# Performance work log

Measured on AMD Instinct MI355X. Metric: run time of the kernel, lower is better.

The kernel has to match this reference:

```python
import jax, jax.numpy as jnp
import numpy as np

B, S, H = 2, 2048, 4096
NH, NKV, HD = 32, 8, 128
THETA = 1000000.0
NEG = jnp.finfo(jnp.float32).min


def setup_inputs() -> dict:
    key = jax.random.key(0)
    ks = jax.random.split(key, 9)
    s = 0.02
    return {
        "hidden_states": jax.random.normal(ks[0], (B, S, H), jnp.float32),
        "position_ids": jnp.tile(jnp.arange(S, dtype=jnp.int32)[None, :], (B, 1)),
        "Wq": jax.random.normal(ks[1], (NH * HD, H), jnp.float32) * s,
        "bq": jax.random.normal(ks[2], (NH * HD,), jnp.float32) * s,
        "Wk": jax.random.normal(ks[3], (NKV * HD, H), jnp.float32) * s,
        "bk": jax.random.normal(ks[4], (NKV * HD,), jnp.float32) * s,
        "Wv": jax.random.normal(ks[5], (NKV * HD, H), jnp.float32) * s,
        "bv": jax.random.normal(ks[6], (NKV * HD,), jnp.float32) * s,
        "Wo": jax.random.normal(ks[7], (H, H), jnp.float32) * s,
        "bo": jax.random.normal(ks[8], (H,), jnp.float32) * s,
    }


def _rotate_half_interleaved(x):
    # y[..., ::2] = -x[..., 1::2]; y[..., 1::2] = x[..., ::2]
    x2 = x.reshape(*x.shape[:-1], -1, 2)
    y = jnp.stack([-x2[..., 1], x2[..., 0]], axis=-1)
    return y.reshape(x.shape)


def reference(hidden_states, position_ids, Wq, bq, Wk, bk, Wv, bv, Wo, bo):
    bsz, q_len, _ = hidden_states.shape
    q = (hidden_states @ Wq.T + bq).reshape(bsz, q_len, NH, HD).transpose(0, 2, 1, 3)
    k = (hidden_states @ Wk.T + bk).reshape(bsz, q_len, NKV, HD).transpose(0, 2, 1, 3)
    v = (hidden_states @ Wv.T + bv).reshape(bsz, q_len, NKV, HD).transpose(0, 2, 1, 3)

    # rotary embedding (interleaved / repeat_interleave variant)
    inv_freq = 1.0 / (THETA ** (jnp.arange(0, HD, 2, dtype=jnp.float32) / HD))
    freqs = position_ids.astype(jnp.float32)[:, :, None] * inv_freq[None, None, :]  # [B,S,HD/2]
    emb = jnp.repeat(freqs, 2, axis=-1)  # [B,S,HD]
    cos = jnp.cos(emb)[:, None, :, :]  # [B,1,S,HD]
    sin = jnp.sin(emb)[:, None, :, :]
    q = q * cos + _rotate_half_interleaved(q) * sin
    k = k * cos + _rotate_half_interleaved(k) * sin

    # GQA: repeat KV heads (repeat_interleave on head axis)
    n_rep = NH // NKV
    k = jnp.repeat(k, n_rep, axis=1)
    v = jnp.repeat(v, n_rep, axis=1)

    scores = jnp.einsum("bhqd,bhkd->bhqk", q, k) / np.sqrt(HD).astype(np.float32)
    causal = jnp.tril(jnp.ones((q_len, q_len), dtype=bool))
    scores = jnp.where(causal[None, None, :, :], scores, NEG)
    attn = jax.nn.softmax(scores.astype(jnp.float32), axis=-1).astype(q.dtype)
    out = jnp.einsum("bhqk,bhkd->bhqd", attn, v)
    out = out.transpose(0, 2, 1, 3).reshape(bsz, q_len, H)
    return out @ Wo.T + bo
```

## Files before the change

### kernel.cpp

```cpp
#include <hip/hip_runtime.h>
#include <stdint.h>

typedef __bf16 bf16x8 __attribute__((ext_vector_type(8)));
typedef float f32x4 __attribute__((ext_vector_type(4)));
typedef float f32x16 __attribute__((ext_vector_type(16)));

#define S_LEN 2048
#define NKVH 8
#define HDIM 128
#define MROWS 4096
#define LDQKV 6144
#define SCALE 0.08838834764831845f
#define C_LOG2 0.1275405707067851f
#define THR_RAW 62.7f
#define ROPE_L2 0.31143075889569023f

__device__ __forceinline__ unsigned short f2bf(float f) {
  unsigned u = __float_as_uint(f);
  u += 0x7FFFu + ((u >> 16) & 1u);
  return (unsigned short)(u >> 16);
}
__device__ __forceinline__ float bf2f(unsigned short h) {
  return __uint_as_float(((unsigned)h) << 16);
}

__device__ __forceinline__ void gload16(const unsigned short* g, unsigned short* l) {
  __builtin_amdgcn_global_load_lds(
      (__attribute__((address_space(1))) void*)(g),
      (__attribute__((address_space(3))) void*)(l), 16, 0, 0);
}

__global__ void cast4(const float4* __restrict__ s0, const float4* __restrict__ s1,
                      const float4* __restrict__ s2, const float4* __restrict__ s3,
                      ushort4* __restrict__ d0, ushort4* __restrict__ d1,
                      ushort4* __restrict__ d2, ushort4* __restrict__ d3) {
  const int b = blockIdx.x;
  const float4* s; ushort4* d; int lb;
  if (b < 1024)      { s = s0; d = d0; lb = b; }
  else if (b < 2048) { s = s1; d = d1; lb = b - 1024; }
  else if (b < 2304) { s = s2; d = d2; lb = b - 2048; }
  else               { s = s3; d = d3; lb = b - 2304; }
  int base = lb * 4096 + threadIdx.x;
#pragma unroll
  for (int i = 0; i < 16; i++) {
    float4 v = s[base + i * 256];
    ushort4 o;
    o.x = f2bf(v.x); o.y = f2bf(v.y); o.z = f2bf(v.z); o.w = f2bf(v.w);
    d[base + i * 256] = o;
  }
}

__global__ void cast_f32_bf16(const float4* __restrict__ in, ushort4* __restrict__ out, int n4) {
  int i = blockIdx.x * 256 + threadIdx.x;
  const int stride = gridDim.x * 256;
  for (; i < n4; i += stride) {
    float4 v = in[i];
    ushort4 o;
    o.x = f2bf(v.x); o.y = f2bf(v.y); o.z = f2bf(v.z); o.w = f2bf(v.w);
    out[i] = o;
  }
}

template <int OUTF, int ROPE>
__global__ __launch_bounds__(512, 2)
void gemm256(const unsigned short* __restrict__ A,
             const unsigned short* __restrict__ Bw,
             const float* __restrict__ bias,
             void* __restrict__ C,
             const int* __restrict__ pos,
             int ldc, int K) {
  __shared__ unsigned short lds[8][8192];

  const int t = threadIdx.x;
  const int lane = t & 63;
  const int w = t >> 6;
  const int wr = w >> 2, wc = w & 3;
  const int row16 = lane & 15, kgrp = lane >> 4;
  const int m0 = blockIdx.y * 256, n0 = blockIdx.x * 256;

  const int riu = t >> 3;
  const int col = (((t & 7) ^ (riu & 7)) << 3);
  const int rB0 = (riu & 31) + ((riu >> 5) << 6);
  const unsigned short* pA = A + (size_t)(m0 + riu) * K + col;
  const unsigned short* pB = Bw + (size_t)(n0 + rB0) * K + col;

#define STGU(SL, SRC)                                                       \
  {                                                                         \
    gload16((SRC), &lds[SL][t * 8]);                                        \
    gload16((SRC) + (size_t)128 * K, &lds[SL][4096 + t * 8]);               \
  }
#define RDA(SL)                                                             \
  _Pragma("unroll") for (int mi = 0; mi < 4; mi++)                          \
  _Pragma("unroll") for (int ks = 0; ks < 2; ks++)                          \
    afr[mi][ks] = *(const bf16x8*)(&lds[SL][0] + abase + mi * 1024 +        \
                                   ((((ks << 2) + kgrp) ^ sw) << 3));
#define RDB(SL, W)                                                          \
  _Pragma("unroll") for (int nj = 0; nj < 2; nj++)                          \
  _Pragma("unroll") for (int ks = 0; ks < 2; ks++)                          \
    bfr[W][nj][ks] = *(const bf16x8*)(&lds[SL][0] + bbase + nj * 1024 +     \
                                      ((((ks << 2) + kgrp) ^ sw) << 3));
#define MM(MO, NO, W)                                                       \
  __builtin_amdgcn_s_setprio(1);                                            \
  _Pragma("unroll") for (int mi = 0; mi < 4; mi++)                          \
  _Pragma("unroll") for (int nj = 0; nj < 2; nj++)                          \
  _Pragma("unroll") for (int ks = 0; ks < 2; ks++)                          \
    acc[(MO) + mi][(NO) + nj] = __builtin_amdgcn_mfma_f32_16x16x32_bf16(    \
        afr[mi][ks], bfr[W][nj][ks], acc[(MO) + mi][(NO) + nj], 0, 0, 0);   \
  __builtin_amdgcn_s_setprio(0);
#define BAR __builtin_amdgcn_s_barrier()

  const int sw = row16 & 7;
  const int abase = (wr * 64 + row16) * 64;
  const int bbase = (wc * 32 + row16) * 64;

  f32x4 acc[8][4];
#pragma unroll
  for (int i = 0; i < 8; i++)
#pragma unroll
    for (int j = 0; j < 4; j++) acc[i][j] = (f32x4){0.f, 0.f, 0.f, 0.f};

  bf16x8 afr[4][2], bfr[2][2][2];
  const int NT = K >> 6;
  const int NI = NT >> 1;

  STGU(0, pA);
  STGU(1, pB);
  STGU(2, pB + (size_t)32 * K);
  STGU(3, pA + (size_t)64 * K);
  STGU(4, pA + 64);
  STGU(5, pB + 64);
  STGU(6, pB + (size_t)32 * K + 64);
  asm volatile("s_waitcnt vmcnt(6)" ::: "memory");
  BAR;

  for (int I = 0; I < NI; ++I) {
    const size_t k1 = ((size_t)(2 * I + 1)) << 6;
    const size_t k2 = ((size_t)(2 * I + 2)) << 6;
    const size_t k3 = ((size_t)(2 * I + 3)) << 6;
    const bool s2 = (I + 1 < NI);

    RDA(0); RDB(1, 0);
    STGU(7, pA + (size_t)64 * K + k1);
    BAR;
    MM(0, 0, 0);
    BAR;
    RDB(2, 1);
    if (s2) STGU(0, pA + k2);
    BAR;
    MM(0, 2, 1);
    BAR;
    RDA(3);
    if (s2) STGU(1, pB + k2);
    BAR;
    MM(4, 2, 1);
    BAR;
    if (s2) {
      STGU(2, pB + (size_t)32 * K + k2);
      asm volatile("s_waitcnt vmcnt(6)" ::: "memory");
    } else {
      asm volatile("s_waitcnt vmcnt(0)" ::: "memory");
    }
    BAR;
    MM(4, 0, 0);
    BAR;
    RDA(4); RDB(5, 0);
    if (s2) STGU(3, pA + (size_t)64 * K + k2);
    BAR;
    MM(0, 0, 0);
    BAR;
    RDB(6, 1);
    if (s2) STGU(4, pA + k3);
    BAR;
    MM(0, 2, 1);
    BAR;
    RDA(7);
    if (s2) STGU(5, pB + k3);
    BAR;
    MM(4, 2, 1);
    BAR;
    if (s2) {
      STGU(6, pB + (size_t)32 * K + k3);
      asm volatile("s_waitcnt vmcnt(6)" ::: "memory");
    } else {
      asm volatile("s_waitcnt vmcnt(0)" ::: "memory");
    }
    BAR;
    MM(4, 0, 0);
    BAR;
  }
#undef STGU
#undef RDA
#undef RDB
#undef MM
#undef BAR

#pragma unroll
  for (int MI = 0; MI < 8; MI++) {
#pragma unroll
    for (int NJ = 0; NJ < 4; NJ++) {
      const int gr = m0 + wr * 128 + MI * 16 + kgrp * 4;
      const int gc = n0 + wc * 64 + NJ * 16 + row16;
      const float bv = bias[gc];
      if (ROPE) {
        const int hf = (gc & 127) >> 1;
        const float inv = exp2f(-(float)hf * ROPE_L2);
#pragma unroll
        for (int jj = 0; jj < 4; jj++) {
          float v = acc[MI][NJ][jj] + bv;
          float px = __shfl_xor(v, 1);
          float sn, cs;
          __sincosf((float)pos[gr + jj] * inv, &sn, &cs);
          float ov = (gc & 1) ? fmaf(v, cs, px * sn) : fmaf(v, cs, -px * sn);
          ((unsigned short*)C)[(size_t)(gr + jj) * ldc + gc] = f2bf(ov);
        }
      } else {
#pragma unroll
        for (int jj = 0; jj < 4; jj++) {
          float v = acc[MI][NJ][jj] + bv;
          if (OUTF) ((float*)C)[(size_t)(gr + jj) * ldc + gc] = v;
          else ((unsigned short*)C)[(size_t)(gr + jj) * ldc + gc] = f2bf(v);
        }
      }
    }
  }
}

template <int OUTF, int ROPE>
__global__ __launch_bounds__(512, 2)
void gemm128(const unsigned short* __restrict__ A,
             const unsigned short* __restrict__ Bw,
             const float* __restrict__ bias,
             void* __restrict__ C,
             const int* __restrict__ pos,
             int ldc, int K) {
  __shared__ unsigned short lds[3 * 24576];

  const int t = threadIdx.x;
  const int lane = t & 63;
  const int w = t >> 6;
  const int wr = w >> 2, wc = w & 3;
  const int row16 = lane & 15, kgrp = lane >> 4;
  const int m0 = blockIdx.y * 128, n0 = blockIdx.x * 256;

  const int riu = t >> 3;
  const int col = (((t & 7) ^ (riu & 7)) << 3);
  const unsigned short* pA = A + (size_t)(m0 + riu) * K + col;
  const unsigned short* pB = Bw + (size_t)(n0 + riu) * K + col;

#define STG6(bo_, kk_)                                                      \
  {                                                                         \
    gload16(pA + (kk_), &lds[(bo_) + t * 8]);                               \
    gload16(pA + (size_t)64 * K + (kk_), &lds[(bo_) + 4096 + t * 8]);       \
    gload16(pB + (kk_), &lds[(bo_) + 8192 + t * 8]);                        \
    gload16(pB + (size_t)64 * K + (kk_), &lds[(bo_) + 12288 + t * 8]);      \
    gload16(pB + (size_t)128 * K + (kk_), &lds[(bo_) + 16384 + t * 8]);     \
    gload16(pB + (size_t)192 * K + (kk_), &lds[(bo_) + 20480 + t * 8]);     \
  }

  const int sw = row16 & 7;
  const int abase = (wr * 64 + row16) * 64;
  const int bbase = 8192 + (wc * 64 + row16) * 64;

  f32x4 acc[4][4];
#pragma unroll
  for (int i = 0; i < 4; i++)
#pragma unroll
    for (int j = 0; j < 4; j++) acc[i][j] = (f32x4){0.f, 0.f, 0.f, 0.f};

  bf16x8 afr[4][2], bfr[4][2];
  const int NT = K >> 6;

  STG6(0, 0);
  STG6(24576, 64);

  int rbc = 0;
  int rbs = 2;
  for (int T = 0; T < NT; ++T) {
    if (T < NT - 1) { asm volatile("s_waitcnt vmcnt(6)\n\ts_barrier" ::: "memory"); }
    else            { asm volatile("s_waitcnt vmcnt(0)\n\ts_barrier" ::: "memory"); }
    if (T + 2 < NT) STG6(rbs * 24576, (size_t)(T + 2) << 6);
    const unsigned short* Lc = &lds[rbc * 24576];

#pragma unroll
    for (int mi = 0; mi < 4; mi++)
#pragma unroll
      for (int ks = 0; ks < 2; ks++)
        afr[mi][ks] = *(const bf16x8*)(Lc + abase + mi * 1024 + ((((ks << 2) + kgrp) ^ sw) << 3));
#pragma unroll
    for (int nj = 0; nj < 4; nj++)
#pragma unroll
      for (int ks = 0; ks < 2; ks++)
        bfr[nj][ks] = *(const bf16x8*)(Lc + bbase + nj * 1024 + ((((ks << 2) + kgrp) ^ sw) << 3));

    __builtin_amdgcn_s_setprio(1);
#pragma unroll
    for (int mi = 0; mi < 4; mi++)
#pragma unroll
      for (int nj = 0; nj < 4; nj++)
#pragma unroll
        for (int ks = 0; ks < 2; ks++)
          acc[mi][nj] = __builtin_amdgcn_mfma_f32_16x16x32_bf16(afr[mi][ks], bfr[nj][ks], acc[mi][nj], 0, 0, 0);
    __builtin_amdgcn_s_setprio(0);

    rbc++; if (rbc == 3) rbc = 0;
    rbs++; if (rbs == 3) rbs = 0;
  }
#undef STG6

#pragma unroll
  for (int MI = 0; MI < 4; MI++) {
#pragma unroll
    for (int NJ = 0; NJ < 4; NJ++) {
      const int gr = m0 + wr * 64 + MI * 16 + kgrp * 4;
      const int gc = n0 + wc * 64 + NJ * 16 + row16;
      const float bv = bias[gc];
      if (ROPE && gc < 1024) {
        const int hf = (gc & 127) >> 1;
        const float inv = exp2f(-(float)hf * ROPE_L2);
#pragma unroll
        for (int jj = 0; jj < 4; jj++) {
          float v = acc[MI][NJ][jj] + bv;
          float px = __shfl_xor(v, 1);
          float sn, cs;
          __sincosf((float)pos[gr + jj] * inv, &sn, &cs);
          float ov = (gc & 1) ? fmaf(v, cs, px * sn) : fmaf(v, cs, -px * sn);
          ((unsigned short*)C)[(size_t)(gr + jj) * ldc + gc] = f2bf(ov);
        }
      } else {
#pragma unroll
        for (int jj = 0; jj < 4; jj++) {
          float v = acc[MI][NJ][jj] + bv;
          if (OUTF) ((float*)C)[(size_t)(gr + jj) * ldc + gc] = v;
          else ((unsigned short*)C)[(size_t)(gr + jj) * ldc + gc] = f2bf(v);
        }
      }
    }
  }
}

__global__ void transpose_v(const unsigned short* __restrict__ V, int ldv,
                            unsigned short* __restrict__ Vt) {
  __shared__ unsigned short tile[32][40];
  const int t = threadIdx.x;
  const int n0 = blockIdx.x * 32;
  const int m0 = blockIdx.y * 32;
  const int r = t >> 3;
  const int c = (t & 7) << 2;
  const unsigned short* src = V + (size_t)(m0 + r) * ldv + n0 + c;
  ushort4 d = *(const ushort4*)src;
  tile[r][c] = d.x; tile[r][c + 1] = d.y; tile[r][c + 2] = d.z; tile[r][c + 3] = d.w;
  __syncthreads();
  const int b = m0 >> 11;
  unsigned short* dst = Vt + (size_t)(b * 1024 + n0 + r) * 2048 + (m0 & 2047) + c;
  ushort4 o;
  o.x = tile[c][r]; o.y = tile[c + 1][r]; o.z = tile[c + 2][r]; o.w = tile[c + 3][r];
  *(ushort4*)dst = o;
}

__global__ __launch_bounds__(256, 2)
void attn_kernel3(const unsigned short* __restrict__ QKV,
                  const unsigned short* __restrict__ Vt,
                  unsigned short* __restrict__ O) {
  __shared__ unsigned short sK[2 * 2 * 64 * 64];
  __shared__ unsigned short sV[2 * 128 * 64];

  const int t = threadIdx.x;
  const int lane = t & 63;
  const int w = t >> 6;
  const int l31 = lane & 31;
  const int hi = lane >> 5;
  const int bid = blockIdx.x;
  const int g = bid >> 6, bh = bid & 63;
  const int qt = (g < 8) ? (15 - g) : (g - 8);
  const int b = bh >> 5, h = bh & 31;
  const int kh = h >> 2;
  const int q0 = qt << 7;
  const int qw = q0 + w * 32;
  const int qg = qw + l31;

  const int ntiles = (q0 + 128) >> 6;
  const int myTiles = (qw + 95) >> 6;

  const int kr5 = t >> 3;
  const int ksw2 = ((t & 7) ^ (kr5 & 7)) << 3;
  const int vrow0 = t >> 3;
  const int vslot = t & 7;
  const unsigned short* Kp = QKV + (size_t)(b * S_LEN) * LDQKV + 4096 + kh * HDIM;
  const unsigned short* Vp = Vt + (size_t)(b * 1024 + kh * HDIM) * 2048;
  const int vsw = (vslot ^ (vrow0 & 7)) << 3;
  const unsigned short* KpA = Kp + (size_t)kr5 * LDQKV + ksw2;
  const unsigned short* VpA = Vp + (size_t)vrow0 * 2048 + vsw;

#define STAGE(bufi, kv0m)                                                      \
  {                                                                            \
    _Pragma("unroll")                                                          \
    for (int p = 0; p < 4; p++)                                                \
      gload16(KpA + (size_t)((kv0m) + ((p & 1) << 5)) * LDQKV + ((p >> 1) << 6), \
              &sK[(bufi) * 8192 + p * 2048 + t * 8]);                          \
    _Pragma("unroll")                                                          \
    for (int p = 0; p < 4; p++)                                                \
      gload16(VpA + (kv0m) + p * 65536, &sV[(bufi) * 8192 + p * 2048 + t * 8]); \
  }

  bf16x8 qf[8];
  {
    const unsigned short* qb = QKV + (size_t)(b * S_LEN + qw + l31) * LDQKV + h * HDIM + hi * 8;
#pragma unroll
    for (int kd = 0; kd < 8; kd++) qf[kd] = *(const bf16x8*)(qb + kd * 16);
  }

  f32x16 o[4];
#pragma unroll
  for (int nt = 0; nt < 4; nt++)
#pragma unroll
    for (int r = 0; r < 16; r++) o[nt][r] = 0.f;
  float m = -1e30f, lsum = 0.f;

  const int rw7 = (l31 & 7) << 4;
  const int kswz = (hi << 4) ^ rw7;
  const int kbase = l31 << 6;
  const int vbase = l31 * 64;

  STAGE(0, 0);
  int buf = 0;
  for (int it = 0; it < ntiles; ++it) {
    if (it + 1 < ntiles) {
      STAGE(buf ^ 1, (it + 1) << 6);
      asm volatile("s_waitcnt vmcnt(8)" ::: "memory");
    } else {
      asm volatile("s_waitcnt vmcnt(0)" ::: "memory");
    }
    __builtin_amdgcn_s_barrier();

    if (it < myTiles) {
      const unsigned short* sKc = sK + buf * 8192;
      const unsigned short* sVc = sV + buf * 8192;
      const int kv0 = it << 6;

      f32x16 st[2];
#pragma unroll
      for (int r = 0; r < 16; r++) { st[0][r] = 0.f; st[1][r] = 0.f; }
      __builtin_amdgcn_s_setprio(1);
#pragma unroll
      for (int kd = 0; kd < 8; kd++) {
        const int koff = ((kd >> 2) << 12) + ((((kd & 3) << 5) ^ kswz) >> 1);
        bf16x8 k0 = *(const bf16x8*)(sKc + koff + kbase);
        bf16x8 k1 = *(const bf16x8*)(sKc + koff + kbase + 2048);
        st[0] = __builtin_amdgcn_mfma_f32_32x32x16_bf16(k0, qf[kd], st[0], 0, 0, 0);
        st[1] = __builtin_amdgcn_mfma_f32_32x32x16_bf16(k1, qf[kd], st[1], 0, 0, 0);
      }
      __builtin_amdgcn_s_setprio(0);

      if (it == myTiles - 1) {
#pragma unroll
        for (int s2 = 0; s2 < 2; s2++)
#pragma unroll
          for (int r = 0; r < 16; r++) {
            const int kvg = kv0 + s2 * 32 + (r & 3) + 8 * (r >> 2) + 4 * hi;
            if (kvg > qg) st[s2][r] = -1e30f;
          }
      }

      float mx[8];
#pragma unroll
      for (int r = 0; r < 8; r++)
        mx[r] = fmaxf(fmaxf(st[0][r], st[0][r + 8]), fmaxf(st[1][r], st[1][r + 8]));
#pragma unroll
      for (int d = 4; d >= 1; d >>= 1)
#pragma unroll
        for (int r = 0; r < d; r++) mx[r] = fmaxf(mx[r], mx[r + d]);
      float tmax = fmaxf(mx[0], __shfl_xor(mx[0], 32));

      if (!__all(tmax <= m + THR_RAW)) {
        const float mnew = fmaxf(m, tmax);
        const float corr = exp2f((m - mnew) * C_LOG2);
        lsum *= corr;
#pragma unroll
        for (int r = 0; r < 16; r++) {
          const int src = (r & 3) + 8 * (r >> 2) + 4 * hi;
          const float cr = __shfl(corr, src);
#pragma unroll
          for (int nt = 0; nt < 4; nt++) o[nt][r] *= cr;
        }
        m = mnew;
      }
      const float mC = m * C_LOG2;

#pragma unroll
      for (int s2 = 0; s2 < 2; s2++)
#pragma unroll
        for (int r = 0; r < 16; r++) st[s2][r] = exp2f(fmaf(st[s2][r], C_LOG2, -mC));
      float sm[8];
#pragma unroll
      for (int r = 0; r < 8; r++)
        sm[r] = (st[0][r] + st[0][r + 8]) + (st[1][r] + st[1][r + 8]);
#pragma unroll
      for (int d = 4; d >= 1; d >>= 1)
#pragma unroll
        for (int r = 0; r < d; r++) sm[r] += sm[r + d];
      float tsum = sm[0] + __shfl_xor(sm[0], 32);
      lsum += tsum;

      bf16x8 pa[4];
#pragma unroll
      for (int s2 = 0; s2 < 2; s2++) {
        unsigned pw[8];
#pragma unroll
        for (int i = 0; i < 8; i++)
          asm("v_cvt_pk_bf16_f32 %0, %1, %2" : "=v"(pw[i]) : "v"(st[s2][2 * i]), "v"(st[s2][2 * i + 1]));
        const unsigned y0 = hi ? pw[0] : pw[2];
        const unsigned y1 = hi ? pw[1] : pw[3];
        const unsigned y2 = hi ? pw[4] : pw[6];
        const unsigned y3 = hi ? pw[5] : pw[7];
        const unsigned x0 = (unsigned)__shfl_xor((int)y0, 32);
        const unsigned x1 = (unsigned)__shfl_xor((int)y1, 32);
        const unsigned x2 = (unsigned)__shfl_xor((int)y2, 32);
        const unsigned x3 = (unsigned)__shfl_xor((int)y3, 32);
        union { unsigned u[4]; bf16x8 v; } u0, u1;
        u0.u[0] = hi ? x0 : pw[0];
        u0.u[1] = hi ? x1 : pw[1];
        u0.u[2] = hi ? pw[2] : x0;
        u0.u[3] = hi ? pw[3] : x1;
        u1.u[0] = hi ? x2 : pw[4];
        u1.u[1] = hi ? x3 : pw[5];
        u1.u[2] = hi ? pw[6] : x2;
        u1.u[3] = hi ? pw[7] : x3;
        pa[2 * s2] = u0.v; pa[2 * s2 + 1] = u1.v;
      }

      __builtin_amdgcn_s_setprio(1);
#pragma unroll
      for (int nt = 0; nt < 4; nt++) {
        const unsigned short* vr = sVc + vbase + nt * 2048;
#pragma unroll
        for (int ks = 0; ks < 4; ks++) {
          bf16x8 vb = *(const bf16x8*)(vr + (((ks << 5) ^ kswz) >> 1));
          o[nt] = __builtin_amdgcn_mfma_f32_32x32x16_bf16(pa[ks], vb, o[nt], 0, 0, 0);
        }
      }
      __builtin_amdgcn_s_setprio(0);
    }

    __builtin_amdgcn_s_barrier();
    buf ^= 1;
  }

  const float linv = 1.0f / lsum;
#pragma unroll
  for (int r = 0; r < 16; r++) {
    const int qr = (r & 3) + 8 * (r >> 2) + 4 * hi;
    const float lr = __shfl(linv, qr);
    unsigned short* orow = O + (size_t)(b * S_LEN + qw + qr) * 4096 + h * HDIM + l31;
#pragma unroll
    for (int nt = 0; nt < 4; nt++) orow[nt * 32] = f2bf(o[nt][r] * lr);
  }
#undef STAGE
}

extern "C" void kernel_launch(void* const* d_in, const int* in_sizes, int n_in,
                              void* d_out, int out_size, void* d_ws, size_t ws_size,
                              hipStream_t stream) {
  const float* hs = (const float*)d_in[0];
  const int*  pos = (const int*)d_in[1];
  const float* Wq = (const float*)d_in[2];
  const float* bq = (const float*)d_in[3];
  const float* Wk = (const float*)d_in[4];
  const float* bk = (const float*)d_in[5];
  const float* Wv = (const float*)d_in[6];
  const float* bv = (const float*)d_in[7];
  const float* Wo = (const float*)d_in[8];
  const float* bo = (const float*)d_in[9];
  float* out = (float*)d_out;

  char* ws = (char*)d_ws;
  unsigned short* hbf  = (unsigned short*)(ws);
  unsigned short* Wbuf = (unsigned short*)(ws + 33554432);
  unsigned short* QKV  = (unsigned short*)(ws + 83886080);
  unsigned short* Vtb  = (unsigned short*)(ws + 134217728);
  float*          biasb= (float*)(ws + 142606336);

  cast4<<<2560, 256, 0, stream>>>(
      (const float4*)hs, (const float4*)Wq, (const float4*)Wk, (const float4*)Wv,
      (ushort4*)hbf, (ushort4*)Wbuf, (ushort4*)(Wbuf + 16777216), (ushort4*)(Wbuf + 20971520));
  hipMemcpyAsync(biasb, bq, 4096 * 4, hipMemcpyDeviceToDevice, stream);
  hipMemcpyAsync(biasb + 4096, bk, 1024 * 4, hipMemcpyDeviceToDevice, stream);
  hipMemcpyAsync(biasb + 5120, bv, 1024 * 4, hipMemcpyDeviceToDevice, stream);

  gemm256<0, 1><<<dim3(16, 16), 512, 0, stream>>>(hbf, Wbuf, biasb, QKV, pos, LDQKV, 4096);
  gemm128<0, 1><<<dim3(8, 32), 512, 0, stream>>>(hbf, Wbuf + 16777216, biasb + 4096, QKV + 4096, pos, LDQKV, 4096);

  cast_f32_bf16<<<2048, 256, 0, stream>>>((const float4*)Wo, (ushort4*)Wbuf, 4194304);

  transpose_v<<<dim3(32, 128), 256, 0, stream>>>(QKV + 5120, LDQKV, Vtb);

  attn_kernel3<<<dim3(1024), 256, 0, stream>>>(QKV, Vtb, hbf);

  gemm256<1, 0><<<dim3(16, 16), 512, 0, stream>>>(hbf, Wbuf, bo, out, nullptr, 4096, 4096);
}
```

Measured before the change: 507.0 us.

## Widen attention KV tile to 128 and drop double-buffered prefetch

The attention kernel now processes 128 keys per iteration instead of 64, using four score accumulators and eight PV k-steps, which halves the loop trips, barriers and softmax rescale passes. To fit the larger tile in the same shared memory, the double buffer is removed, so each tile is loaded and then waited on with vmcnt(0) before compute. This gives up the overlap of global loads with compute, and the coarser causal tiles do more wasted masked work on diagonal blocks.

```diff
diff --git a/kernel.cpp b/kernel.cpp
--- a/kernel.cpp
+++ b/kernel.cpp
@@ -358,10 +358,10 @@
 }
 
 __global__ __launch_bounds__(256, 2)
-void attn_kernel3(const unsigned short* __restrict__ QKV,
+void attn_kernel4(const unsigned short* __restrict__ QKV,
                   const unsigned short* __restrict__ Vt,
                   unsigned short* __restrict__ O) {
-  __shared__ unsigned short sK[2 * 2 * 64 * 64];
+  __shared__ unsigned short sK[2 * 128 * 64];
   __shared__ unsigned short sV[2 * 128 * 64];
 
   const int t = threadIdx.x;
@@ -378,28 +378,26 @@
   const int qw = q0 + w * 32;
   const int qg = qw + l31;
 
-  const int ntiles = (q0 + 128) >> 6;
-  const int myTiles = (qw + 95) >> 6;
-
-  const int kr5 = t >> 3;
-  const int ksw2 = ((t & 7) ^ (kr5 & 7)) << 3;
-  const int vrow0 = t >> 3;
-  const int vslot = t & 7;
+  const int ntiles = qt + 1;
+  const int myTiles = (qw + 159) >> 7;
+
+  const int r5 = t >> 3;
+  const int psw = ((t & 7) ^ (r5 & 7)) << 3;
   const unsigned short* Kp = QKV + (size_t)(b * S_LEN) * LDQKV + 4096 + kh * HDIM;
   const unsigned short* Vp = Vt + (size_t)(b * 1024 + kh * HDIM) * 2048;
-  const int vsw = (vslot ^ (vrow0 & 7)) << 3;
-  const unsigned short* KpA = Kp + (size_t)kr5 * LDQKV + ksw2;
-  const unsigned short* VpA = Vp + (size_t)vrow0 * 2048 + vsw;
-
-#define STAGE(bufi, kv0m)                                                      \
+  const unsigned short* KpA = Kp + (size_t)r5 * LDQKV + psw;
+  const unsigned short* VpA = Vp + (size_t)r5 * 2048 + psw;
+
+#define STAGE(kv0m)                                                            \
   {                                                                            \
     _Pragma("unroll")                                                          \
-    for (int p = 0; p < 4; p++)                                                \
-      gload16(KpA + (size_t)((kv0m) + ((p & 1) << 5)) * LDQKV + ((p >> 1) << 6), \
-              &sK[(bufi) * 8192 + p * 2048 + t * 8]);                          \
+    for (int p = 0; p < 8; p++)                                                \
+      gload16(KpA + (size_t)((kv0m) + ((p & 3) << 5)) * LDQKV + ((p >> 2) << 6), \
+              &sK[p * 2048 + t * 8]);                                          \
     _Pragma("unroll")                                                          \
-    for (int p = 0; p < 4; p++)                                                \
-      gload16(VpA + (kv0m) + p * 65536, &sV[(bufi) * 8192 + p * 2048 + t * 8]); \
+    for (int p = 0; p < 8; p++)                                                \
+      gload16(VpA + (size_t)((p & 3) << 5) * 2048 + (kv0m) + ((p >> 2) << 6),  \
+              &sV[p * 2048 + t * 8]);                                          \
   }
 
   bf16x8 qf[8];
@@ -418,42 +416,37 @@
 
   const int rw7 = (l31 & 7) << 4;
   const int kswz = (hi << 4) ^ rw7;
-  const int kbase = l31 << 6;
-  const int vbase = l31 * 64;
-
-  STAGE(0, 0);
-  int buf = 0;
+  const int rbase = l31 << 6;
+
   for (int it = 0; it < ntiles; ++it) {
-    if (it + 1 < ntiles) {
-      STAGE(buf ^ 1, (it + 1) << 6);
-      asm volatile("s_waitcnt vmcnt(8)" ::: "memory");
-    } else {
-      asm volatile("s_waitcnt vmcnt(0)" ::: "memory");
-    }
+    STAGE(it << 7);
+    asm volatile("s_waitcnt vmcnt(0)" ::: "memory");
     __builtin_amdgcn_s_barrier();
 
     if (it < myTiles) {
-      const unsigned short* sKc = sK + buf * 8192;
-      const unsigned short* sVc = sV + buf * 8192;
-      const int kv0 = it << 6;
-
-      f32x16 st[2];
-#pragma unroll
-      for (int r = 0; r < 16; r++) { st[0][r] = 0.f; st[1][r] = 0.f; }
+      const int kv0 = it << 7;
+
+      f32x16 st[4];
+#pragma unroll
+      for (int r = 0; r < 16; r++) { st[0][r] = 0.f; st[1][r] = 0.f; st[2][r] = 0.f; st[3][r] = 0.f; }
       __builtin_amdgcn_s_setprio(1);
 #pragma unroll
       for (int kd = 0; kd < 8; kd++) {
-        const int koff = ((kd >> 2) << 12) + ((((kd & 3) << 5) ^ kswz) >> 1);
-        bf16x8 k0 = *(const bf16x8*)(sKc + koff + kbase);
-        bf16x8 k1 = *(const bf16x8*)(sKc + koff + kbase + 2048);
+        const int koff = ((kd >> 2) << 13) + ((((kd & 3) << 5) ^ kswz) >> 1);
+        bf16x8 k0 = *(const bf16x8*)(sK + koff + rbase);
+        bf16x8 k1 = *(const bf16x8*)(sK + koff + rbase + 2048);
+        bf16x8 k2 = *(const bf16x8*)(sK + koff + rbase + 4096);
+        bf16x8 k3 = *(const bf16x8*)(sK + koff + rbase + 6144);
         st[0] = __builtin_amdgcn_mfma_f32_32x32x16_bf16(k0, qf[kd], st[0], 0, 0, 0);
         st[1] = __builtin_amdgcn_mfma_f32_32x32x16_bf16(k1, qf[kd], st[1], 0, 0, 0);
+        st[2] = __builtin_amdgcn_mfma_f32_32x32x16_bf16(k2, qf[kd], st[2], 0, 0, 0);
+        st[3] = __builtin_amdgcn_mfma_f32_32x32x16_bf16(k3, qf[kd], st[3], 0, 0, 0);
       }
       __builtin_amdgcn_s_setprio(0);
 
       if (it == myTiles - 1) {
 #pragma unroll
-        for (int s2 = 0; s2 < 2; s2++)
+        for (int s2 = 0; s2 < 4; s2++)
 #pragma unroll
           for (int r = 0; r < 16; r++) {
             const int kvg = kv0 + s2 * 32 + (r & 3) + 8 * (r >> 2) + 4 * hi;
@@ -464,7 +457,8 @@
       float mx[8];
 #pragma unroll
       for (int r = 0; r < 8; r++)
-        mx[r] = fmaxf(fmaxf(st[0][r], st[0][r + 8]), fmaxf(st[1][r], st[1][r + 8]));
+        mx[r] = fmaxf(fmaxf(fmaxf(st[0][r], st[0][r + 8]), fmaxf(st[1][r], st[1][r + 8])),
+                      fmaxf(fmaxf(st[2][r], st[2][r + 8]), fmaxf(st[3][r], st[3][r + 8])));
 #pragma unroll
       for (int d = 4; d >= 1; d >>= 1)
 #pragma unroll
@@ -487,13 +481,14 @@
       const float mC = m * C_LOG2;
 
 #pragma unroll
-      for (int s2 = 0; s2 < 2; s2++)
+      for (int s2 = 0; s2 < 4; s2++)
 #pragma unroll
         for (int r = 0; r < 16; r++) st[s2][r] = exp2f(fmaf(st[s2][r], C_LOG2, -mC));
       float sm[8];
 #pragma unroll
       for (int r = 0; r < 8; r++)
-        sm[r] = (st[0][r] + st[0][r + 8]) + (st[1][r] + st[1][r + 8]);
+        sm[r] = ((st[0][r] + st[0][r + 8]) + (st[1][r] + st[1][r + 8])) +
+                ((st[2][r] + st[2][r + 8]) + (st[3][r] + st[3][r + 8]));
 #pragma unroll
       for (int d = 4; d >= 1; d >>= 1)
 #pragma unroll
@@ -501,9 +496,9 @@
       float tsum = sm[0] + __shfl_xor(sm[0], 32);
       lsum += tsum;
 
-      bf16x8 pa[4];
-#pragma unroll
-      for (int s2 = 0; s2 < 2; s2++) {
+      bf16x8 pa[8];
+#pragma unroll
+      for (int s2 = 0; s2 < 4; s2++) {
         unsigned pw[8];
 #pragma unroll
         for (int i = 0; i < 8; i++)
@@ -531,10 +526,10 @@
       __builtin_amdgcn_s_setprio(1);
 #pragma unroll
       for (int nt = 0; nt < 4; nt++) {
-        const unsigned short* vr = sVc + vbase + nt * 2048;
-#pragma unroll
-        for (int ks = 0; ks < 4; ks++) {
-          bf16x8 vb = *(const bf16x8*)(vr + (((ks << 5) ^ kswz) >> 1));
+        const unsigned short* vr = sV + nt * 2048 + rbase;
+#pragma unroll
+        for (int ks = 0; ks < 8; ks++) {
+          bf16x8 vb = *(const bf16x8*)(vr + ((ks >> 2) << 13) + ((((ks & 3) << 5) ^ kswz) >> 1));
           o[nt] = __builtin_amdgcn_mfma_f32_32x32x16_bf16(pa[ks], vb, o[nt], 0, 0, 0);
         }
       }
@@ -542,7 +537,6 @@
     }
 
     __builtin_amdgcn_s_barrier();
-    buf ^= 1;
   }
 
   const float linv = 1.0f / lsum;
@@ -593,7 +587,7 @@
 
   transpose_v<<<dim3(32, 128), 256, 0, stream>>>(QKV + 5120, LDQKV, Vtb);
 
-  attn_kernel3<<<dim3(1024), 256, 0, stream>>>(QKV, Vtb, hbf);
+  attn_kernel4<<<dim3(1024), 256, 0, stream>>>(QKV, Vtb, hbf);
 
   gemm256<1, 0><<<dim3(16, 16), 512, 0, stream>>>(hbf, Wbuf, bo, out, nullptr, 4096, 4096);
 }
```

After: 506.0 us. Within noise of the previous version (-0.2%).
